# Kernel optimization log

Hardware: AMD Instinct MI355X
Metric: run time of the kernel (lower is better)

Reference implementation:

```python
import jax, jax.numpy as jnp
import numpy as np

N = 50000        # nodes
E_RAND = 800000  # random edges; self-loops appended -> E = E_RAND + N
H = 4            # heads
D_IN = 256
D_HID = 64       # per-head hidden (H*D_HID == D_IN -> identity residual in layer 1)
D_OUT = 32       # classes per head
SLOPE = 0.2      # leaky-relu negative slope


def setup_inputs() -> dict:
    key = jax.random.key(0)
    ks = jax.random.split(key, 13)
    loops = jnp.arange(N, dtype=jnp.int32)
    src = jnp.concatenate([jax.random.randint(ks[0], (E_RAND,), 0, N, dtype=jnp.int32), loops])
    dst = jnp.concatenate([jax.random.randint(ks[1], (E_RAND,), 0, N, dtype=jnp.int32), loops])
    h = jax.random.normal(ks[2], (N, D_IN), dtype=jnp.float32)
    def w(k, shape, fan):
        return jax.random.normal(k, shape, dtype=jnp.float32) * (1.0 / np.sqrt(fan))
    return {
        "h": h, "src": src, "dst": dst,
        # layer 1 (tuple in_feats -> separate fc_src / fc_dst in dgl GATConv)
        "W1_src": w(ks[3], (D_IN, H * D_HID), D_IN),
        "W1_dst": w(ks[4], (D_IN, H * D_HID), D_IN),
        "al1": w(ks[5], (H, D_HID), D_HID),
        "ar1": w(ks[6], (H, D_HID), D_HID),
        # layer 2
        "W2_src": w(ks[7], (H * D_HID, H * D_OUT), H * D_HID),
        "W2_dst": w(ks[8], (H * D_HID, H * D_OUT), H * D_HID),
        "al2": w(ks[9], (H, D_OUT), D_OUT),
        "ar2": w(ks[10], (H, D_OUT), D_OUT),
        # residual projection for layer 2 (in_dim != heads*out)
        "Wres2": w(ks[11], (H * D_HID, H * D_OUT), H * D_HID),
    }


def gat_conv(h_node, src, dst, Ws, Wd, al, ar, heads, dout, resval):
    n = h_node.shape[0]
    fs = (h_node @ Ws).reshape(n, heads, dout)   # [N,H,D] projected src feats
    fd = (h_node @ Wd).reshape(n, heads, dout)
    el = jnp.sum(fs * al, axis=-1)               # [N,H]
    er = jnp.sum(fd * ar, axis=-1)               # [N,H]
    e = jax.nn.leaky_relu(el[src] + er[dst], SLOPE)           # [E,H] edge scores
    emax = jax.ops.segment_max(e, dst, num_segments=n)        # segment softmax over dst
    ex = jnp.exp(e - emax[dst])
    denom = jax.ops.segment_sum(ex, dst, num_segments=n)
    a = ex / denom[dst]                                        # [E,H] attention
    msg = fs[src] * a[:, :, None]                              # [E,H,D] gather * weight
    out = jax.ops.segment_sum(msg, dst, num_segments=n)       # [N,H,D] scatter-add
    return out + resval


def reference(h, src, dst, W1_src, W1_dst, al1, ar1, W2_src, W2_dst, al2, ar2, Wres2):
    # layer 1: identity residual (in_dim == heads*hidden), elu activation, flatten heads
    res1 = h.reshape(-1, H, D_HID)
    h1 = gat_conv(h, src, dst, W1_src, W1_dst, al1, ar1, H, D_HID, res1)
    h1 = jax.nn.elu(h1).reshape(-1, H * D_HID)
    # layer 2: linear residual, no activation, mean over heads
    res2 = (h1 @ Wres2).reshape(-1, H, D_OUT)
    h2 = gat_conv(h1, src, dst, W2_src, W2_dst, al2, ar2, H, D_OUT, res2)
    return h2.mean(axis=1)                                     # [N, num_classes]
```

## Files before the change

### kernel.cpp

```cpp
#include <hip/hip_runtime.h>
#include <hip/hip_bf16.h>

#define NN 50000
#define EE 850000
#define NBLK_SCAN 98

typedef unsigned short u16;
using short8 = __attribute__((ext_vector_type(8))) short;
using f32x4  = __attribute__((ext_vector_type(4))) float;

__device__ __forceinline__ float bf2f(u16 u) {
    union { unsigned int i; float f; } v; v.i = ((unsigned int)u) << 16; return v.f;
}
__device__ __forceinline__ u16 f2bf(float f) {
    __hip_bfloat16 h = __float2bfloat16(f);
    return *reinterpret_cast<u16*>(&h);
}

__device__ __forceinline__ float ld1(const void* X, size_t i, bool f32m) {
    return f32m ? ((const float*)X)[i] : bf2f(((const u16*)X)[i]);
}
__device__ __forceinline__ void load4(const void* X, size_t g, bool f32m, float o[4]) {
    if (f32m) {
        float4 v = ((const float4*)X)[g];
        o[0] = v.x; o[1] = v.y; o[2] = v.z; o[3] = v.w;
    } else {
        ushort4 v = ((const ushort4*)X)[g];
        o[0] = bf2f(v.x); o[1] = bf2f(v.y); o[2] = bf2f(v.z); o[3] = bf2f(v.w);
    }
}

__global__ void k_detect(const u16* __restrict__ hh, int* __restrict__ flag,
                         int* __restrict__ deg) {
    if (blockIdx.x != 0) {
        int i = (blockIdx.x - 1) * 256 + threadIdx.x;
        if (i < NN) deg[i] = 0;
        return;
    }
    __shared__ int sm[256];
    int t = threadIdx.x;
    int c = 0;
    for (int i = 0; i < 16; ++i) {
        u16 u = hh[t * 16 + i];
        int e = (u >> 7) & 0xFF;
        if (e != 0 && (e < 90 || e > 160)) ++c;
    }
    sm[t] = c;
    __syncthreads();
    for (int s = 128; s > 0; s >>= 1) {
        if (t < s) sm[t] += sm[t + s];
        __syncthreads();
    }
    if (t == 0) *flag = (sm[0] > 200) ? 1 : 0;
}

__global__ void k_prep(const void* __restrict__ W1s, const void* __restrict__ al1,
                       const void* __restrict__ W1d, const void* __restrict__ ar1,
                       const void* __restrict__ W2s, const void* __restrict__ al2,
                       const void* __restrict__ W2d, const void* __restrict__ ar2,
                       const void* __restrict__ Wres2, const int* __restrict__ dst,
                       u16* __restrict__ BT1, u16* __restrict__ BT2,
                       float* __restrict__ wl1, float* __restrict__ wr1,
                       float* __restrict__ wl2, float* __restrict__ wr2,
                       int* __restrict__ deg, int* __restrict__ eorder,
                       const int* __restrict__ mode) {
    int bid = blockIdx.x;
    if (bid >= 528) {
        int e = (bid - 528) * 256 + threadIdx.x;
        if (e < EE) {
            int r = atomicAdd(&deg[dst[e]], 1);
            eorder[e] = r;
        }
        return;
    }
    bool f32m = (*mode) != 0;
    if (bid < 512) {
        int id = bid * 256 + threadIdx.x;
        int which = id >> 16;
        int rem = id & 65535;
        int n = rem >> 8, k = rem & 255;
        if (which == 0) {
            BT1[n * 256 + k] = f2bf(ld1(W1s, (size_t)k * 256 + n, f32m));
        } else {
            float v = (n < 128) ? ld1(W2s, (size_t)k * 128 + n, f32m)
                                : ld1(Wres2, (size_t)k * 128 + (n - 128), f32m);
            BT2[n * 256 + k] = f2bf(v);
        }
    } else {
        int id = (bid - 512) * 256 + threadIdx.x;
        int which = id >> 10;
        int rem = id & 1023;
        int k = rem >> 2, h = rem & 3;
        float s = 0.f;
        if (which == 0) {
            for (int d = 0; d < 64; ++d) s += ld1(W1s, k * 256 + h * 64 + d, f32m) * ld1(al1, h * 64 + d, f32m);
            wl1[k * 4 + h] = s;
        } else if (which == 1) {
            for (int d = 0; d < 64; ++d) s += ld1(W1d, k * 256 + h * 64 + d, f32m) * ld1(ar1, h * 64 + d, f32m);
            wr1[k * 4 + h] = s;
        } else if (which == 2) {
            for (int d = 0; d < 32; ++d) s += ld1(W2s, k * 128 + h * 32 + d, f32m) * ld1(al2, h * 32 + d, f32m);
            wl2[k * 4 + h] = s;
        } else {
            for (int d = 0; d < 32; ++d) s += ld1(W2d, k * 128 + h * 32 + d, f32m) * ld1(ar2, h * 32 + d, f32m);
            wr2[k * 4 + h] = s;
        }
    }
}

__global__ void k_scan1(const int* __restrict__ deg, int* __restrict__ rowptr,
                        int* __restrict__ bsum) {
    __shared__ int sm[512];
    int t = threadIdx.x;
    int i = blockIdx.x * 512 + t;
    int v = (i < NN) ? deg[i] : 0;
    int x = v;
    sm[t] = x;
    __syncthreads();
    for (int off = 1; off < 512; off <<= 1) {
        int y = (t >= off) ? sm[t - off] : 0;
        __syncthreads();
        x += y;
        sm[t] = x;
        __syncthreads();
    }
    if (i < NN) rowptr[i] = x - v;
    if (t == 511) bsum[blockIdx.x] = x;
}

__global__ void k_scan3_eler1(int* __restrict__ rowptr, const int* __restrict__ bsum,
                              const void* __restrict__ X, u16* __restrict__ hb,
                              const float* __restrict__ wl, const float* __restrict__ wr,
                              float* __restrict__ el, float* __restrict__ er,
                              const int* __restrict__ mode) {
    int bid = blockIdx.x;
    if (bid < 196) {
        __shared__ int sm[NBLK_SCAN];
        int t = threadIdx.x;
        if (t < NBLK_SCAN) sm[t] = bsum[t];
        __syncthreads();
        int g = bid >> 1;
        int pre = 0;
        for (int j = 0; j < g; ++j) pre += sm[j];
        int i = bid * 256 + t;
        if (i < NN) {
            rowptr[i] += pre;
            if (i == 0) rowptr[NN] = EE;
        }
        return;
    }
    bool f32m = (*mode) != 0;
    int wave = threadIdx.x >> 6, lane = threadIdx.x & 63;
    int node = (bid - 196) * 4 + wave;
    float a[4];
    load4(X, (size_t)node * 64 + lane, f32m, a);
    ushort4 hv = {f2bf(a[0]), f2bf(a[1]), f2bf(a[2]), f2bf(a[3])};
    ((ushort4*)hb)[(size_t)node * 64 + lane] = hv;
    float accl[4] = {0, 0, 0, 0}, accr[4] = {0, 0, 0, 0};
    int k0 = lane * 4;
#pragma unroll
    for (int j = 0; j < 4; ++j) {
        float4 wlv = ((const float4*)wl)[k0 + j];
        float4 wrv = ((const float4*)wr)[k0 + j];
        accl[0] += a[j] * wlv.x; accl[1] += a[j] * wlv.y;
        accl[2] += a[j] * wlv.z; accl[3] += a[j] * wlv.w;
        accr[0] += a[j] * wrv.x; accr[1] += a[j] * wrv.y;
        accr[2] += a[j] * wrv.z; accr[3] += a[j] * wrv.w;
    }
#pragma unroll
    for (int off = 32; off > 0; off >>= 1) {
#pragma unroll
        for (int t = 0; t < 4; ++t) {
            accl[t] += __shfl_down(accl[t], off, 64);
            accr[t] += __shfl_down(accr[t], off, 64);
        }
    }
    if (lane == 0) {
        float4 vl = {accl[0], accl[1], accl[2], accl[3]};
        float4 vr = {accr[0], accr[1], accr[2], accr[3]};
        ((float4*)el)[node] = vl;
        ((float4*)er)[node] = vr;
    }
}

__global__ void k_awgen(const int* __restrict__ src, const int* __restrict__ dst,
                        const int* __restrict__ eorder, const int* __restrict__ rowptr,
                        const float* __restrict__ el, const float* __restrict__ er,
                        uint4* __restrict__ meta) {
    int e = blockIdx.x * 256 + threadIdx.x;
    if (e >= EE) return;
    int s = src[e], d = dst[e];
    int slot = rowptr[d] + eorder[e];
    float4 eL = ((const float4*)el)[s];
    float4 eR = ((const float4*)er)[d];
    float ev[4] = {eL.x + eR.x, eL.y + eR.y, eL.z + eR.z, eL.w + eR.w};
    u16 op[4];
#pragma unroll
    for (int t = 0; t < 4; ++t) {
        float x = ev[t];
        x = x > 0.f ? x : 0.2f * x;
        x = fminf(fmaxf(x, -60.f), 60.f);
        op[t] = f2bf(__expf(x));
    }
    uint4 m;
    m.x = (unsigned int)s;
    m.y = (unsigned int)op[0] | ((unsigned int)op[1] << 16);
    m.z = (unsigned int)op[2] | ((unsigned int)op[3] << 16);
    m.w = 0u;
    meta[slot] = m;
}

__global__ void k_gemm_mfma(const u16* __restrict__ A,
                            const u16* __restrict__ BT, u16* __restrict__ C) {
    __shared__ u16 smem[128 * 72 * 2];
    u16* At = smem;
    u16* Bt = smem + 128 * 72;
    int t = threadIdx.x;
    int lane = t & 63, w = t >> 6;
    int mt = blockIdx.x >> 1, nt = blockIdx.x & 1;
    int m0 = mt * 128, n0 = nt * 128;
    int wr = (w >> 1) * 64, wc = (w & 1) * 64;
    f32x4 acc[4][4] = {};
    int q = lane >> 4, cl = lane & 15;

    for (int ph = 0; ph < 4; ++ph) {
        int kb = ph * 64;
        for (int it = 0; it < 4; ++it) {
            int c = it * 256 + t;
            int row = c >> 3, c8 = c & 7;
            int rowg = m0 + row;
            float4 av;
            if (rowg < NN) {
                av = *(const float4*)(A + (size_t)rowg * 256 + kb + c8 * 8);
            } else {
                av = make_float4(0.f, 0.f, 0.f, 0.f);
            }
            *(float4*)&At[row * 72 + c8 * 8] = av;
            float4 bv = *(const float4*)(BT + (size_t)(n0 + row) * 256 + kb + c8 * 8);
            *(float4*)&Bt[row * 72 + c8 * 8] = bv;
        }
        __syncthreads();
#pragma unroll
        for (int ks = 0; ks < 2; ++ks) {
            short8 af[4], bf[4];
#pragma unroll
            for (int i = 0; i < 4; ++i)
                af[i] = *(const short8*)&At[(wr + i * 16 + cl) * 72 + ks * 32 + q * 8];
#pragma unroll
            for (int j = 0; j < 4; ++j)
                bf[j] = *(const short8*)&Bt[(wc + j * 16 + cl) * 72 + ks * 32 + q * 8];
#pragma unroll
            for (int i = 0; i < 4; ++i)
#pragma unroll
                for (int j = 0; j < 4; ++j)
                    acc[i][j] = __builtin_amdgcn_mfma_f32_16x16x32_bf16(af[i], bf[j], acc[i][j], 0, 0, 0);
        }
        __syncthreads();
    }
    u16* Ct = smem;
    int sw_w = q << 1;
#pragma unroll
    for (int i = 0; i < 4; ++i)
#pragma unroll
        for (int j = 0; j < 4; ++j) {
            int colb = wc + j * 16 + cl;
            int chunk = (colb >> 3) ^ sw_w;
#pragma unroll
            for (int r = 0; r < 4; ++r) {
                int row = wr + i * 16 + q * 4 + r;
                Ct[row * 128 + chunk * 8 + (colb & 7)] = f2bf(acc[i][j][r]);
            }
        }
    __syncthreads();
#pragma unroll
    for (int it = 0; it < 8; ++it) {
        int c = it * 256 + t;
        int row = c >> 4, k16 = c & 15;
        int mrow = m0 + row;
        if (mrow < NN) {
            int phys = k16 ^ (((row >> 2) & 3) << 1);
            float4 v = *(const float4*)&Ct[row * 128 + phys * 8];
            *(float4*)&C[(size_t)mrow * 256 + n0 + k16 * 8] = v;
        }
    }
}

__global__ void k_agg1(const int* __restrict__ rowptr, const uint4* __restrict__ meta,
                       const u16* __restrict__ fs, u16* __restrict__ hb,
                       const float* __restrict__ wl2, const float* __restrict__ wr2,
                       float* __restrict__ el2, float* __restrict__ er2) {
    int wave = threadIdx.x >> 6, lane = threadIdx.x & 63;
    int node = blockIdx.x * 4 + wave;
    int beg = rowptr[node], end = rowptr[node + 1];
    int head = lane >> 4;
    int hs2 = head & 2, hs1 = head & 1;
    float a0 = 0.f, a1 = 0.f, a2 = 0.f, a3 = 0.f, ll = 0.f;
#pragma unroll 8
    for (int p = beg; p < end; ++p) {
        uint4 mv = meta[p];
        int s = (int)mv.x;
        unsigned int wp = hs2 ? mv.z : mv.y;
        float pw = bf2f(hs1 ? (u16)(wp >> 16) : (u16)wp);
        ushort4 fv = *(const ushort4*)(fs + (size_t)s * 256 + lane * 4);
        ll += pw;
        a0 += pw * bf2f(fv.x);
        a1 += pw * bf2f(fv.y);
        a2 += pw * bf2f(fv.z);
        a3 += pw * bf2f(fv.w);
    }
    float rinv = 1.f / ll;
    ushort4 rv = ((const ushort4*)hb)[(size_t)node * 64 + lane];
    float v0 = a0 * rinv + bf2f(rv.x), v1 = a1 * rinv + bf2f(rv.y);
    float v2 = a2 * rinv + bf2f(rv.z), v3 = a3 * rinv + bf2f(rv.w);
    v0 = v0 > 0.f ? v0 : __expf(v0) - 1.f;
    v1 = v1 > 0.f ? v1 : __expf(v1) - 1.f;
    v2 = v2 > 0.f ? v2 : __expf(v2) - 1.f;
    v3 = v3 > 0.f ? v3 : __expf(v3) - 1.f;
    ushort4 o = {f2bf(v0), f2bf(v1), f2bf(v2), f2bf(v3)};
    ((ushort4*)hb)[(size_t)node * 64 + lane] = o;
    float4 w0 = ((const float4*)wl2)[lane * 4 + 0];
    float4 w1 = ((const float4*)wl2)[lane * 4 + 1];
    float4 w2 = ((const float4*)wl2)[lane * 4 + 2];
    float4 w3 = ((const float4*)wl2)[lane * 4 + 3];
    float4 r0 = ((const float4*)wr2)[lane * 4 + 0];
    float4 r1 = ((const float4*)wr2)[lane * 4 + 1];
    float4 r2 = ((const float4*)wr2)[lane * 4 + 2];
    float4 r3 = ((const float4*)wr2)[lane * 4 + 3];
    float acl[4], acr[4];
    acl[0] = v0 * w0.x + v1 * w1.x + v2 * w2.x + v3 * w3.x;
    acl[1] = v0 * w0.y + v1 * w1.y + v2 * w2.y + v3 * w3.y;
    acl[2] = v0 * w0.z + v1 * w1.z + v2 * w2.z + v3 * w3.z;
    acl[3] = v0 * w0.w + v1 * w1.w + v2 * w2.w + v3 * w3.w;
    acr[0] = v0 * r0.x + v1 * r1.x + v2 * r2.x + v3 * r3.x;
    acr[1] = v0 * r0.y + v1 * r1.y + v2 * r2.y + v3 * r3.y;
    acr[2] = v0 * r0.z + v1 * r1.z + v2 * r2.z + v3 * r3.z;
    acr[3] = v0 * r0.w + v1 * r1.w + v2 * r2.w + v3 * r3.w;
#pragma unroll
    for (int off = 32; off > 0; off >>= 1) {
#pragma unroll
        for (int t = 0; t < 4; ++t) {
            acl[t] += __shfl_down(acl[t], off, 64);
            acr[t] += __shfl_down(acr[t], off, 64);
        }
    }
    if (lane == 0) {
        float4 vl = {acl[0], acl[1], acl[2], acl[3]};
        float4 vr = {acr[0], acr[1], acr[2], acr[3]};
        ((float4*)el2)[node] = vl;
        ((float4*)er2)[node] = vr;
    }
}

__global__ void k_agg2(const int* __restrict__ rowptr, const uint4* __restrict__ meta,
                       const u16* __restrict__ c2,
                       void* __restrict__ out, const int* __restrict__ mode) {
    bool f32m = (*mode) != 0;
    int wave = threadIdx.x >> 6, lane = threadIdx.x & 63;
    int node = blockIdx.x * 4 + wave;
    int beg = rowptr[node], end = rowptr[node + 1];
    int head = lane >> 4;
    int hs2 = head & 2, hs1 = head & 1;
    float a0 = 0.f, a1 = 0.f, ll = 0.f;
#pragma unroll 8
    for (int p = beg; p < end; ++p) {
        uint4 mv = meta[p];
        int s = (int)mv.x;
        unsigned int wp = hs2 ? mv.z : mv.y;
        float pw = bf2f(hs1 ? (u16)(wp >> 16) : (u16)wp);
        ushort2 fv = *(const ushort2*)(c2 + (size_t)s * 256 + lane * 2);
        ll += pw;
        a0 += pw * bf2f(fv.x);
        a1 += pw * bf2f(fv.y);
    }
    float rinv = 1.f / ll;
    ushort2 rv = *(const ushort2*)(c2 + (size_t)node * 256 + 128 + lane * 2);
    float o0 = a0 * rinv + bf2f(rv.x);
    float o1 = a1 * rinv + bf2f(rv.y);
    o0 += __shfl_xor(o0, 16, 64); o0 += __shfl_xor(o0, 32, 64);
    o1 += __shfl_xor(o1, 16, 64); o1 += __shfl_xor(o1, 32, 64);
    if (lane < 16) {
        float v0 = 0.25f * o0, v1 = 0.25f * o1;
        size_t oi = (size_t)node * 32 + lane * 2;
        if (f32m) {
            ((float*)out)[oi] = v0;
            ((float*)out)[oi + 1] = v1;
        } else {
            ushort2 ov = {f2bf(v0), f2bf(v1)};
            *(ushort2*)((u16*)out + oi) = ov;
        }
    }
}

extern "C" void kernel_launch(void* const* d_in, const int* in_sizes, int n_in,
                              void* d_out, int out_size, void* d_ws, size_t ws_size,
                              hipStream_t stream) {
    int ih = 0, isrc = 1, idst = 2, iW1s = 3, iW1d = 4, ial1 = 5, iar1 = 6,
        iW2s = 7, iW2d = 8, ial2 = 9, iar2 = 10, iWres = 11;
    if (n_in >= 12 && in_sizes[0] != 12800000) {
        iW1d = 0; iW1s = 1; iW2d = 2; iW2s = 3; iWres = 4; ial1 = 5; ial2 = 6;
        iar1 = 7; iar2 = 8; idst = 9; ih = 10; isrc = 11;
    }
    const void* h     = d_in[ih];
    const int* src    = (const int*)d_in[isrc];
    const int* dst    = (const int*)d_in[idst];
    const void* W1s   = d_in[iW1s];
    const void* W1d   = d_in[iW1d];
    const void* al1   = d_in[ial1];
    const void* ar1   = d_in[iar1];
    const void* W2s   = d_in[iW2s];
    const void* W2d   = d_in[iW2d];
    const void* al2   = d_in[ial2];
    const void* ar2   = d_in[iar2];
    const void* Wres2 = d_in[iWres];

    char* w = (char*)d_ws;
    size_t off = 0;
    auto alloc = [&](size_t bytes) -> void* {
        void* p = w + off;
        off += (bytes + 255) & ~(size_t)255;
        return p;
    };
    int* mode   = (int*)alloc(256);
    float* wl1 = (float*)alloc(256 * 4 * 4);
    float* wr1 = (float*)alloc(256 * 4 * 4);
    float* wl2 = (float*)alloc(256 * 4 * 4);
    float* wr2 = (float*)alloc(256 * 4 * 4);
    int* deg    = (int*)alloc(NN * 4);
    int* rowptr = (int*)alloc((NN + 1) * 4);
    int* bsum   = (int*)alloc(NBLK_SCAN * 4);
    int* eorder = (int*)alloc((size_t)EE * 4);
    uint4* meta = (uint4*)alloc((size_t)EE * 16);
    float* el1  = (float*)alloc((size_t)NN * 4 * 4);
    float* er1  = (float*)alloc((size_t)NN * 4 * 4);
    float* el2  = (float*)alloc((size_t)NN * 4 * 4);
    float* er2  = (float*)alloc((size_t)NN * 4 * 4);
    u16* BT1    = (u16*)alloc(256 * 256 * 2);
    u16* BT2    = (u16*)alloc(256 * 256 * 2);
    u16* fs1    = (u16*)alloc((size_t)NN * 256 * 2);
    u16* hb     = (u16*)alloc((size_t)NN * 256 * 2);
    u16* c2     = fs1;

    k_detect<<<197, 256, 0, stream>>>((const u16*)h, mode, deg);
    k_prep<<<528 + (EE + 255) / 256, 256, 0, stream>>>(
        W1s, al1, W1d, ar1, W2s, al2, W2d, ar2, Wres2, dst,
        BT1, BT2, wl1, wr1, wl2, wr2, deg, eorder, mode);
    k_scan1<<<NBLK_SCAN, 512, 0, stream>>>(deg, rowptr, bsum);
    k_scan3_eler1<<<196 + NN / 4, 256, 0, stream>>>(rowptr, bsum,
                                                    h, hb, wl1, wr1, el1, er1, mode);
    k_awgen<<<(EE + 255) / 256, 256, 0, stream>>>(src, dst, eorder, rowptr,
                                                  el1, er1, meta);
    k_gemm_mfma<<<782, 256, 0, stream>>>(hb, BT1, fs1);
    k_agg1<<<NN / 4, 256, 0, stream>>>(rowptr, meta, fs1, hb,
                                       wl2, wr2, el2, er2);
    k_gemm_mfma<<<782, 256, 0, stream>>>(hb, BT2, c2);
    k_awgen<<<(EE + 255) / 256, 256, 0, stream>>>(src, dst, eorder, rowptr,
                                                  el2, er2, meta);
    k_agg2<<<NN / 4, 256, 0, stream>>>(rowptr, meta, c2, d_out, mode);
}
```

Before: 377.2 us.

## Fuse layer-2 attention weight computation into aggregation, drop second edge-weight pass

Removes the second edge-weight generation pass over all edges. Layer-2 aggregation now recomputes the leaky-relu and exp weights on the fly from el2[src] and er2[dst], reading only the source index from the existing CSR metadata. Layer-1 aggregation loads the source index and the per-head bf16 weight as scalar loads instead of a full uint4 plus branchy selection. In exchange, agg2 does extra gathers of el2 and more exp work per edge per lane. The layer-2 weights also stay in fp32 rather than being rounded to bf16.

```diff
diff --git a/kernel.cpp b/kernel.cpp
--- a/kernel.cpp
+++ b/kernel.cpp
@@ -183,7 +183,7 @@
     }
 }
 
-__global__ void k_awgen(const int* __restrict__ src, const int* __restrict__ dst,
+__global__ void k_scatw(const int* __restrict__ src, const int* __restrict__ dst,
                         const int* __restrict__ eorder, const int* __restrict__ rowptr,
                         const float* __restrict__ el, const float* __restrict__ er,
                         uint4* __restrict__ meta) {
@@ -293,14 +293,13 @@
     int node = blockIdx.x * 4 + wave;
     int beg = rowptr[node], end = rowptr[node + 1];
     int head = lane >> 4;
-    int hs2 = head & 2, hs1 = head & 1;
+    const int* ms = (const int*)meta;
+    const u16* mw = (const u16*)meta + 2 + head;
     float a0 = 0.f, a1 = 0.f, a2 = 0.f, a3 = 0.f, ll = 0.f;
 #pragma unroll 8
     for (int p = beg; p < end; ++p) {
-        uint4 mv = meta[p];
-        int s = (int)mv.x;
-        unsigned int wp = hs2 ? mv.z : mv.y;
-        float pw = bf2f(hs1 ? (u16)(wp >> 16) : (u16)wp);
+        int s = ms[(size_t)p * 4];
+        float pw = bf2f(mw[(size_t)p * 8]);
         ushort4 fv = *(const ushort4*)(fs + (size_t)s * 256 + lane * 4);
         ll += pw;
         a0 += pw * bf2f(fv.x);
@@ -352,6 +351,7 @@
 }
 
 __global__ void k_agg2(const int* __restrict__ rowptr, const uint4* __restrict__ meta,
+                       const float* __restrict__ el2, const float* __restrict__ er2,
                        const u16* __restrict__ c2,
                        void* __restrict__ out, const int* __restrict__ mode) {
     bool f32m = (*mode) != 0;
@@ -359,14 +359,16 @@
     int node = blockIdx.x * 4 + wave;
     int beg = rowptr[node], end = rowptr[node + 1];
     int head = lane >> 4;
-    int hs2 = head & 2, hs1 = head & 1;
+    const int* ms = (const int*)meta;
+    float erh = er2[node * 4 + head];
     float a0 = 0.f, a1 = 0.f, ll = 0.f;
 #pragma unroll 8
     for (int p = beg; p < end; ++p) {
-        uint4 mv = meta[p];
-        int s = (int)mv.x;
-        unsigned int wp = hs2 ? mv.z : mv.y;
-        float pw = bf2f(hs1 ? (u16)(wp >> 16) : (u16)wp);
+        int s = ms[(size_t)p * 4];
+        float x = el2[s * 4 + head] + erh;
+        x = x > 0.f ? x : 0.2f * x;
+        x = fminf(fmaxf(x, -60.f), 60.f);
+        float pw = __expf(x);
         ushort2 fv = *(const ushort2*)(c2 + (size_t)s * 256 + lane * 2);
         ll += pw;
         a0 += pw * bf2f(fv.x);
@@ -447,13 +449,11 @@
     k_scan1<<<NBLK_SCAN, 512, 0, stream>>>(deg, rowptr, bsum);
     k_scan3_eler1<<<196 + NN / 4, 256, 0, stream>>>(rowptr, bsum,
                                                     h, hb, wl1, wr1, el1, er1, mode);
-    k_awgen<<<(EE + 255) / 256, 256, 0, stream>>>(src, dst, eorder, rowptr,
+    k_scatw<<<(EE + 255) / 256, 256, 0, stream>>>(src, dst, eorder, rowptr,
                                                   el1, er1, meta);
     k_gemm_mfma<<<782, 256, 0, stream>>>(hb, BT1, fs1);
     k_agg1<<<NN / 4, 256, 0, stream>>>(rowptr, meta, fs1, hb,
                                        wl2, wr2, el2, er2);
     k_gemm_mfma<<<782, 256, 0, stream>>>(hb, BT2, c2);
-    k_awgen<<<(EE + 255) / 256, 256, 0, stream>>>(src, dst, eorder, rowptr,
-                                                  el2, er2, meta);
-    k_agg2<<<NN / 4, 256, 0, stream>>>(rowptr, meta, c2, d_out, mode);
-}
+    k_agg2<<<NN / 4, 256, 0, stream>>>(rowptr, meta, el2, er2, c2, d_out, mode);
+}
```

Result: faster. 354.6 us (-6.0%).
